# Optimization experiments

Hardware: AMD Instinct MI355X
Metric: run time of the kernel (lower is better)

The kernel has to match this reference:

```python
import jax, jax.numpy as jnp
import numpy as np

B, O, N = 8, 100, 4096
TOK_D, D, K, H = 2048, 256, 128, 8
DH = D // H
LN_EPS = 1e-5


def _ln(x, g, b):
    m = x.mean(-1, keepdims=True)
    v = ((x - m) ** 2).mean(-1, keepdims=True)
    return (x - m) * jax.lax.rsqrt(v + LN_EPS) * g + b


def setup_inputs() -> dict:
    key = jax.random.key(0)
    ks = jax.random.split(key, 16)
    s = 0.02
    return {
        "activation": jax.random.uniform(ks[0], (B, O, N), jnp.float32),
        "tokens": jax.random.normal(ks[1], (B, N, TOK_D), jnp.float32),
        "W_tok": jax.random.normal(ks[2], (TOK_D, D), jnp.float32) * s,
        "b_tok": jnp.zeros((D,), jnp.float32),
        "g_tn": jnp.ones((D,), jnp.float32),
        "bt_tn": jnp.zeros((D,), jnp.float32),
        "pool_query": jax.random.normal(ks[3], (D,), jnp.float32) * s,
        "Wq": jax.random.normal(ks[4], (D, D), jnp.float32) * s,
        "bq": jnp.zeros((D,), jnp.float32),
        "Wk": jax.random.normal(ks[5], (D, D), jnp.float32) * s,
        "bk": jnp.zeros((D,), jnp.float32),
        "Wv": jax.random.normal(ks[6], (D, D), jnp.float32) * s,
        "bv": jnp.zeros((D,), jnp.float32),
        "Wo": jax.random.normal(ks[7], (D, D), jnp.float32) * s,
        "bo": jnp.zeros((D,), jnp.float32),
        "g_pn": jnp.ones((D,), jnp.float32),
        "bt_pn": jnp.zeros((D,), jnp.float32),
        "g_on": jnp.ones((D,), jnp.float32),
        "bt_on": jnp.zeros((D,), jnp.float32),
    }


def reference(activation, tokens, W_tok, b_tok, g_tn, bt_tn, pool_query,
              Wq, bq, Wk, bk, Wv, bv, Wo, bo, g_pn, bt_pn, g_on, bt_on):
    # project + norm the shared token pool: [B, N, D]
    tp = _ln(tokens @ W_tok + b_tok, g_tn, bt_tn)

    # weighted-average branch
    w = activation / jnp.clip(activation.sum(-1, keepdims=True), 1e-8)
    weighted_avg = jnp.einsum('bon,bnd->bod', w, tp)

    # top-k attention branch
    _, topk_idx = jax.lax.top_k(activation, K)            # [B, O, K]
    topk_tokens = jax.vmap(lambda t, i: t[i])(tp, topk_idx)  # [B, O, K, D]

    # MultiheadAttention with a single shared query vector (q_len = 1)
    q = (pool_query @ Wq + bq).reshape(H, DH)             # [H, DH]
    kp = (topk_tokens @ Wk + bk).reshape(B, O, K, H, DH)
    vp = (topk_tokens @ Wv + bv).reshape(B, O, K, H, DH)
    scores = jnp.einsum('hd,bokhd->bohk', q, kp) / np.sqrt(DH).astype(np.float32)
    attn = jax.nn.softmax(scores, axis=-1)                # [B, O, H, K]
    pooled = jnp.einsum('bohk,bokhd->bohd', attn, vp).reshape(B, O, D)
    pooled = _ln(pooled @ Wo + bo, g_pn, bt_pn)

    return _ln(weighted_avg + pooled, g_on, bt_on)
```

## Files before the change

kernel.cpp:

```cpp
#include <hip/hip_runtime.h>
#include <hip/hip_bf16.h>

#define DEVI static __device__ __forceinline__

typedef __attribute__((ext_vector_type(8))) short short8;
typedef __attribute__((ext_vector_type(4))) float f32x4;

#define B_   8
#define O_   100
#define N_   4096
#define TOKD 2048
#define D_   256
#define K_   128
#define H_   8
#define M_   (B_*N_)

DEVI unsigned short f2bf(float f) {
    unsigned u = __float_as_uint(f);
    u = (u + 0x7FFFu + ((u >> 16) & 1u)) >> 16;
    return (unsigned short)u;
}
DEVI float bf2f(unsigned v) { return __uint_as_float(v << 16); }

DEVI unsigned pkbf(float lo, float hi) {
    unsigned r;
    asm("v_cvt_pk_bf16_f32 %0, %1, %2" : "=v"(r) : "v"(lo), "v"(hi));
    return r;
}
DEVI void gload16(const void* g, void* l) {
    __builtin_amdgcn_global_load_lds((const __attribute__((address_space(1))) void*)g,
                                     (__attribute__((address_space(3))) void*)l, 16, 0, 0);
}

__global__ __launch_bounds__(256) void k_pre(const float* __restrict__ act,
                                             int* __restrict__ oidx,
                                             float* __restrict__ asum,
                                             const float* __restrict__ W,
                                             unsigned short* __restrict__ wtb,
                                             const float* __restrict__ pq,
                                             const float* __restrict__ Wq,
                                             const float* __restrict__ bqv,
                                             const float* __restrict__ Wk,
                                             const float* __restrict__ bkv,
                                             float* __restrict__ qW,
                                             float* __restrict__ qb) {
    __shared__ __align__(16) char smem[50304];
    const int t = threadIdx.x, lane = t & 63, wid = t >> 6;

    if (blockIdx.x >= 800) {
        const int bx = blockIdx.x - 800;
        if (bx < 2048) {
            int idx = bx * 256 + t;
            int k = idx >> 8, n = idx & 255;
            wtb[n * TOKD + k] = f2bf(W[idx]);
            return;
        }
        float (*qpart)[32] = (float(*)[32])smem;
        float* qhl = (float*)(smem + 1024);
        const int h = bx - 2048;
        const int col = h * 32 + (t & 31), sl = t >> 5;
        float s = 0.f;
        #pragma unroll
        for (int e = 0; e < 32; ++e) s += pq[sl * 32 + e] * Wq[(sl * 32 + e) * D_ + col];
        qpart[sl][t & 31] = s;
        __syncthreads();
        if (t < 32) {
            float u = bqv[h * 32 + t];
            #pragma unroll
            for (int s8 = 0; s8 < 8; ++s8) u += qpart[s8][t];
            qhl[t] = u;
        }
        __syncthreads();
        float u = 0.f;
        #pragma unroll
        for (int dd = 0; dd < 32; ++dd) u += qhl[dd] * Wk[t * D_ + h * 32 + dd];
        qW[h * D_ + t] = u;
        if (t == 0) {
            float z = 0.f;
            for (int dd = 0; dd < 32; ++dd) z += qhl[dd] * bkv[h * 32 + dd];
            qb[h] = z;
        }
        return;
    }

    int* hist = (int*)smem;
    unsigned long long* cand = (unsigned long long*)(smem + 16384);
    int* csum = (int*)(smem + 49152);
    int* sb   = (int*)(smem + 50192);
    int* cnts = (int*)(smem + 50200);
    float* redf = (float*)(smem + 50208);
    unsigned long long* redu = (unsigned long long*)(smem + 50224);

    const int blk = blockIdx.x;
    const float* rp = act + (size_t)blk * N_;
    float fv[16]; unsigned vb[16]; int bins[16];
    float fs = 0.f;
    #pragma unroll
    for (int i = 0; i < 16; ++i) {
        float f = rp[t + i * 256];
        fv[i] = f; vb[i] = __float_as_uint(f);
        fs += f;
    }
    #pragma unroll
    for (int i = 0; i < 16; ++i) hist[t + i * 256] = 0;
    if (t == 0) { cnts[0] = 0; cnts[1] = 0; }
    #pragma unroll
    for (int m = 1; m < 64; m <<= 1) fs += __shfl_xor(fs, m);
    if (!lane) redf[wid] = fs;
    __syncthreads();
    if (t == 0) asum[blk] = fmaxf(redf[0] + redf[1] + redf[2] + redf[3], 1e-8f);

    #pragma unroll
    for (int i = 0; i < 16; ++i) {
        float f = fv[i];
        int b = (f >= 1.0f) ? 4095 : ((f > 0.f) ? (int)(f * 4096.f) : 0);
        bins[i] = b;
        atomicAdd(&hist[b], 1);
    }
    __syncthreads();

    int cs = 0;
    #pragma unroll
    for (int i = 0; i < 16; ++i) cs += hist[t * 16 + i];
    int v = cs;
    #pragma unroll
    for (int off = 1; off < 64; off <<= 1) {
        int o = __shfl_down(v, off);
        if (lane + off < 64) v += o;
    }
    if (!lane) csum[256 + wid] = v;
    __syncthreads();
    int stot = 0;
    for (int w2 = wid + 1; w2 < 4; ++w2) stot += csum[256 + w2];
    int suff = v + stot;
    csum[t] = suff;
    __syncthreads();
    int nxtc = (t < 255) ? csum[t + 1] : 0;
    if (suff >= K_ && nxtc < K_) {
        int run = nxtc, bstar = t * 16;
        for (int bi = 15; bi >= 0; --bi) {
            run += hist[t * 16 + bi];
            if (run >= K_) { bstar = t * 16 + bi; break; }
        }
        sb[0] = bstar;
    }
    __syncthreads();
    const int bstar = sb[0];

    #pragma unroll
    for (int i = 0; i < 16; ++i) {
        if (bins[i] > bstar) {
            int p = atomicAdd(&cnts[0], 1);
            oidx[blk * K_ + p] = t + i * 256;
        } else if (bins[i] == bstar) {
            int p = atomicAdd(&cnts[1], 1);
            cand[p] = ((unsigned long long)vb[i] << 16) | (unsigned)(4095 - (t + i * 256));
        }
    }
    __syncthreads();
    const int g = cnts[0], E = cnts[1], m = K_ - g;
    unsigned long long last = ~0ull;
    for (int slot = 0; slot < m; ++slot) {
        unsigned long long best = 0;
        for (int i = t; i < E; i += 256) {
            unsigned long long e = cand[i];
            if (e < last && e > best) best = e;
        }
        #pragma unroll
        for (int mm = 1; mm < 64; mm <<= 1) {
            unsigned long long o = __shfl_xor(best, mm);
            if (o > best) best = o;
        }
        if (!lane) redu[wid] = best;
        __syncthreads();
        best = redu[0];
        if (redu[1] > best) best = redu[1];
        if (redu[2] > best) best = redu[2];
        if (redu[3] > best) best = redu[3];
        if (t == 0) oidx[blk * K_ + g + slot] = 4095 - (int)(best & 0xFFFFull);
        last = best;
        __syncthreads();
    }
}

__global__ __launch_bounds__(512, 2) void k_gemm1(const float* __restrict__ A,
                                                  const unsigned short* __restrict__ Bt,
                                                  const float* __restrict__ btok,
                                                  const float* __restrict__ g,
                                                  const float* __restrict__ bt,
                                                  unsigned short* __restrict__ tp) {
    __shared__ __align__(16) char smem[98304];
    const int t = threadIdx.x;
    const int bm = blockIdx.x;
    const int lane = t & 63, w = t >> 6;
    const int wm = w >> 2, wn = w & 3;
    const int lr = lane >> 4, lc = lane & 15;

    const int arow = t >> 2;
    const int acb = (t & 3) * 32;
    const float* agp = A + (size_t)(bm * 128 + arow) * TOKD + (t & 3) * 16;
    const int aw0 = arow * 128 + (acb ^ ((arow & 7) << 4));
    const int aw1 = arow * 128 + ((acb + 16) ^ ((arow & 7) << 4));
    const unsigned short* bg = Bt + (size_t)(t >> 3) * TOKD
                        + (((((t & 7) << 4)) ^ (((t >> 3) & 7) << 4)) >> 1);
    char* bldsw = smem + 32768 + (t >> 6) * 1024;

    f32x4 acc[4][4] = {};
    const int NT = TOKD / 64;
    float4 a0, a1, a2, a3;

    a0 = *(const float4*)(agp);     a1 = *(const float4*)(agp + 4);
    a2 = *(const float4*)(agp + 8); a3 = *(const float4*)(agp + 12);
    #pragma unroll
    for (int c = 0; c < 4; ++c) gload16(bg + (size_t)c * 64 * TOKD, bldsw + c * 8192);
    {
        uint4 w0, w1;
        w0.x = pkbf(a0.x, a0.y); w0.y = pkbf(a0.z, a0.w);
        w0.z = pkbf(a1.x, a1.y); w0.w = pkbf(a1.z, a1.w);
        w1.x = pkbf(a2.x, a2.y); w1.y = pkbf(a2.z, a2.w);
        w1.z = pkbf(a3.x, a3.y); w1.w = pkbf(a3.z, a3.w);
        *(uint4*)(smem + aw0) = w0; *(uint4*)(smem + aw1) = w1;
    }
    a0 = *(const float4*)(agp + 64);  a1 = *(const float4*)(agp + 68);
    a2 = *(const float4*)(agp + 72);  a3 = *(const float4*)(agp + 76);
    asm volatile("s_waitcnt vmcnt(4) lgkmcnt(0)" ::: "memory");
    __builtin_amdgcn_s_barrier();

    int cur = 0;
    for (int kt = 0; kt < NT; ++kt) {
        const int nxt = cur ^ 1;
        if (kt + 1 < NT) {
            const unsigned short* bn = bg + (size_t)(kt + 1) * 64;
            #pragma unroll
            for (int c = 0; c < 4; ++c)
                gload16(bn + (size_t)c * 64 * TOKD, bldsw + nxt * 32768 + c * 8192);
        }
        const char* Ab = smem + cur * 16384;
        const char* Bb = smem + 32768 + cur * 32768;
        #pragma unroll
        for (int kk = 0; kk < 2; ++kk) {
            short8 afr[4], bfr[4];
            #pragma unroll
            for (int mi = 0; mi < 4; ++mi) {
                int row = wm * 64 + mi * 16 + lc;
                afr[mi] = *(const short8*)(Ab + row * 128 + ((kk * 64 + lr * 16) ^ ((row & 7) << 4)));
            }
            #pragma unroll
            for (int ni = 0; ni < 4; ++ni) {
                int n = wn * 64 + ni * 16 + lc;
                bfr[ni] = *(const short8*)(Bb + n * 128 + ((kk * 64 + lr * 16) ^ ((n & 7) << 4)));
            }
            __builtin_amdgcn_s_setprio(1);
            #pragma unroll
            for (int mi = 0; mi < 4; ++mi)
                #pragma unroll
                for (int ni = 0; ni < 4; ++ni)
                    acc[mi][ni] = __builtin_amdgcn_mfma_f32_16x16x32_bf16(afr[mi], bfr[ni], acc[mi][ni], 0, 0, 0);
            __builtin_amdgcn_s_setprio(0);
        }
        if (kt + 1 < NT) {
            char* Anw = smem + nxt * 16384;
            uint4 w0, w1;
            w0.x = pkbf(a0.x, a0.y); w0.y = pkbf(a0.z, a0.w);
            w0.z = pkbf(a1.x, a1.y); w0.w = pkbf(a1.z, a1.w);
            w1.x = pkbf(a2.x, a2.y); w1.y = pkbf(a2.z, a2.w);
            w1.z = pkbf(a3.x, a3.y); w1.w = pkbf(a3.z, a3.w);
            *(uint4*)(Anw + aw0) = w0; *(uint4*)(Anw + aw1) = w1;
            if (kt + 2 < NT) {
                const float* ap = agp + (size_t)(kt + 2) * 64;
                a0 = *(const float4*)(ap);     a1 = *(const float4*)(ap + 4);
                a2 = *(const float4*)(ap + 8); a3 = *(const float4*)(ap + 12);
                asm volatile("s_waitcnt vmcnt(4) lgkmcnt(0)" ::: "memory");
            } else {
                asm volatile("s_waitcnt vmcnt(0) lgkmcnt(0)" ::: "memory");
            }
            __builtin_amdgcn_s_barrier();
            cur = nxt;
        }
    }
    __syncthreads();

    float* ep = (float*)smem;
    const int col0 = lane * 4;
    float4 b4 = *(const float4*)(btok + col0);
    float4 g4 = *(const float4*)(g + col0);
    float4 t4 = *(const float4*)(bt + col0);
    #pragma unroll
    for (int chunk = 0; chunk < 2; ++chunk) {
        if (wm == chunk) {
            #pragma unroll
            for (int mi = 0; mi < 4; ++mi)
                #pragma unroll
                for (int ni = 0; ni < 4; ++ni)
                    #pragma unroll
                    for (int r = 0; r < 4; ++r)
                        ep[(mi * 16 + lr * 4 + r) * 260 + wn * 64 + ni * 16 + lc] = acc[mi][ni][r];
        }
        __syncthreads();
        #pragma unroll
        for (int rr = 0; rr < 8; ++rr) {
            int row = w * 8 + rr;
            float4 x4 = *(const float4*)(ep + row * 260 + col0);
            float x0 = x4.x + b4.x, x1 = x4.y + b4.y, x2 = x4.z + b4.z, x3 = x4.w + b4.w;
            float s = x0 + x1 + x2 + x3;
            float q = x0*x0 + x1*x1 + x2*x2 + x3*x3;
            #pragma unroll
            for (int m = 1; m < 64; m <<= 1) { s += __shfl_xor(s, m); q += __shfl_xor(q, m); }
            float mean = s * (1.f/256.f);
            float var = q * (1.f/256.f) - mean * mean;
            float rs = rsqrtf(var + 1e-5f);
            ushort4 o;
            o.x = f2bf((x0-mean)*rs*g4.x + t4.x);
            o.y = f2bf((x1-mean)*rs*g4.y + t4.y);
            o.z = f2bf((x2-mean)*rs*g4.z + t4.z);
            o.w = f2bf((x3-mean)*rs*g4.w + t4.w);
            *(ushort4*)(tp + (size_t)(bm * 128 + chunk * 64 + row) * D_ + col0) = o;
        }
        __syncthreads();
    }
}

__global__ __launch_bounds__(256) void k_wavg(const float* __restrict__ act,
                                              const unsigned short* __restrict__ tp,
                                              float* __restrict__ partial) {
    const int kc = blockIdx.x;
    const int b = blockIdx.y;
    const int d = threadIdx.x;
    const unsigned short* tpb = tp + ((size_t)b * N_ + kc * 128) * D_ + d;
    const float* actb = act + (size_t)b * O_ * N_ + kc * 128;
    float* pout = partial + ((size_t)(b * 32 + kc) * O_) * D_ + d;
    for (int oci = 0; oci < 2; ++oci) {
        const int oc = blockIdx.z * 2 + oci;
        float acc[10] = {};
        #pragma unroll 2
        for (int q = 0; q < 32; ++q) {
            float t0 = bf2f(tpb[(q * 4 + 0) * D_]);
            float t1 = bf2f(tpb[(q * 4 + 1) * D_]);
            float t2 = bf2f(tpb[(q * 4 + 2) * D_]);
            float t3 = bf2f(tpb[(q * 4 + 3) * D_]);
            #pragma unroll
            for (int oj = 0; oj < 10; ++oj) {
                float4 a4 = *(const float4*)(actb + (size_t)(oc * 10 + oj) * N_ + q * 4);
                acc[oj] += a4.x * t0 + a4.y * t1 + a4.z * t2 + a4.w * t3;
            }
        }
        #pragma unroll
        for (int oj = 0; oj < 10; ++oj)
            pout[(size_t)(oc * 10 + oj) * D_] = acc[oj];
    }
}

DEVI int swz(int j, int chunk) { return j * 512 + ((chunk ^ (j & 31)) << 4); }

__global__ __launch_bounds__(256) void k_attn(
    const unsigned short* __restrict__ tp, const int* __restrict__ oidx,
    const float* __restrict__ qW, const float* __restrict__ qbv,
    const float* __restrict__ Wv, const float* __restrict__ bv,
    const float* __restrict__ Wo, const float* __restrict__ bo,
    const float* __restrict__ g_pn, const float* __restrict__ bt_pn,
    const float* __restrict__ g_on, const float* __restrict__ bt_on,
    const float* __restrict__ partial, const float* __restrict__ asum,
    float* __restrict__ outp)
{
    __shared__ uint4 tgU[4096];
    __shared__ float sc[H_ * K_];
    __shared__ float ul[H_ * D_];
    __shared__ float pool_lds[D_];
    __shared__ float redf[8];
    __shared__ int idxl[K_];
    char* tg = (char*)tgU;

    const int t = threadIdx.x, lane = t & 63, wid = t >> 6;
    const int blk = blockIdx.x;
    const int b = blk / O_;
    const int o = blk - b * O_;

    if (t < K_) idxl[t] = oidx[blk * K_ + t];
    __syncthreads();

    #pragma unroll
    for (int it = 0; it < 16; ++it) {
        int c = t + it * 256;
        int j = c >> 5, ch = c & 31;
        uint4 v = *(const uint4*)(tp + ((size_t)(b * N_ + idxl[j])) * D_ + ch * 8);
        *(uint4*)(tg + swz(j, ch)) = v;
    }
    __syncthreads();

    {
        const int j = t & 127, hq = t >> 7;
        const float* q0 = qW + hq * 4 * D_;
        float s0 = 0.f, s1 = 0.f, s2 = 0.f, s3 = 0.f;
        #pragma unroll 4
        for (int e8 = 0; e8 < 32; ++e8) {
            uint4 tv = *(const uint4*)(tg + swz(j, e8));
            float f0 = bf2f(tv.x & 0xffffu), f1 = bf2f(tv.x >> 16);
            float f2 = bf2f(tv.y & 0xffffu), f3 = bf2f(tv.y >> 16);
            float f4 = bf2f(tv.z & 0xffffu), f5 = bf2f(tv.z >> 16);
            float f6 = bf2f(tv.w & 0xffffu), f7 = bf2f(tv.w >> 16);
            const float* qa = q0 + e8 * 8;
            const float* qbp = qa + D_;
            const float* qc = qa + 2 * D_;
            const float* qd = qa + 3 * D_;
            s0 += f0*qa[0]+f1*qa[1]+f2*qa[2]+f3*qa[3]+f4*qa[4]+f5*qa[5]+f6*qa[6]+f7*qa[7];
            s1 += f0*qbp[0]+f1*qbp[1]+f2*qbp[2]+f3*qbp[3]+f4*qbp[4]+f5*qbp[5]+f6*qbp[6]+f7*qbp[7];
            s2 += f0*qc[0]+f1*qc[1]+f2*qc[2]+f3*qc[3]+f4*qc[4]+f5*qc[5]+f6*qc[6]+f7*qc[7];
            s3 += f0*qd[0]+f1*qd[1]+f2*qd[2]+f3*qd[3]+f4*qd[4]+f5*qd[5]+f6*qd[6]+f7*qd[7];
        }
        const float sca = 0.1767766952966369f;
        sc[(hq * 4 + 0) * K_ + j] = (s0 + qbv[hq * 4 + 0]) * sca;
        sc[(hq * 4 + 1) * K_ + j] = (s1 + qbv[hq * 4 + 1]) * sca;
        sc[(hq * 4 + 2) * K_ + j] = (s2 + qbv[hq * 4 + 2]) * sca;
        sc[(hq * 4 + 3) * K_ + j] = (s3 + qbv[hq * 4 + 3]) * sca;
    }
    __syncthreads();

    #pragma unroll
    for (int hh = 0; hh < 2; ++hh) {
        int h = wid * 2 + hh;
        float v0 = sc[h * K_ + lane], v1 = sc[h * K_ + 64 + lane];
        float mx = fmaxf(v0, v1);
        #pragma unroll
        for (int m = 1; m < 64; m <<= 1) mx = fmaxf(mx, __shfl_xor(mx, m));
        float e0 = __expf(v0 - mx), e1 = __expf(v1 - mx);
        float ss = e0 + e1;
        #pragma unroll
        for (int m = 1; m < 64; m <<= 1) ss += __shfl_xor(ss, m);
        float inv = 1.0f / ss;
        sc[h * K_ + lane] = e0 * inv;
        sc[h * K_ + 64 + lane] = e1 * inv;
    }
    __syncthreads();

    {
        const int h = t >> 5, eg = t & 31;
        float a8[8] = {};
        #pragma unroll 2
        for (int jb = 0; jb < 32; ++jb) {
            f32x4 p4 = *(const f32x4*)(sc + h * K_ + jb * 4);
            #pragma unroll
            for (int ji = 0; ji < 4; ++ji) {
                int j = jb * 4 + ji;
                uint4 tv = *(const uint4*)(tg + swz(j, eg));
                float pw = p4[ji];
                a8[0] += pw * bf2f(tv.x & 0xffffu); a8[1] += pw * bf2f(tv.x >> 16);
                a8[2] += pw * bf2f(tv.y & 0xffffu); a8[3] += pw * bf2f(tv.y >> 16);
                a8[4] += pw * bf2f(tv.z & 0xffffu); a8[5] += pw * bf2f(tv.z >> 16);
                a8[6] += pw * bf2f(tv.w & 0xffffu); a8[7] += pw * bf2f(tv.w >> 16);
            }
        }
        #pragma unroll
        for (int i = 0; i < 8; ++i) ul[h * D_ + eg * 8 + i] = a8[i];
    }
    __syncthreads();

    {
        int h = t >> 5;
        const float* up = ul + h * D_;
        float p = bv[t];
        #pragma unroll 8
        for (int e = 0; e < D_; ++e) p += up[e] * Wv[e * D_ + t];
        pool_lds[t] = p;
    }
    __syncthreads();
    float po = bo[t];
    #pragma unroll 8
    for (int e = 0; e < D_; ++e) po += pool_lds[e] * Wo[e * D_ + t];

    float s1 = po, q1 = po * po;
    #pragma unroll
    for (int m = 1; m < 64; m <<= 1) { s1 += __shfl_xor(s1, m); q1 += __shfl_xor(q1, m); }
    if (!lane) { redf[wid] = s1; redf[4 + wid] = q1; }
    __syncthreads();
    s1 = redf[0] + redf[1] + redf[2] + redf[3];
    q1 = redf[4] + redf[5] + redf[6] + redf[7];
    float mean = s1 * (1.f/256.f);
    float var = q1 * (1.f/256.f) - mean * mean;
    float rs = rsqrtf(var + 1e-5f);
    float pl = (po - mean) * rs * g_pn[t] + bt_pn[t];
    __syncthreads();

    float wa = 0.f;
    const float* pp = partial + ((size_t)(b * 32) * O_ + o) * D_ + t;
    #pragma unroll 8
    for (int kc = 0; kc < 32; ++kc) wa += pp[(size_t)kc * O_ * D_];
    float x = wa / asum[blk] + pl;
    float s2 = x, q2 = x * x;
    #pragma unroll
    for (int m = 1; m < 64; m <<= 1) { s2 += __shfl_xor(s2, m); q2 += __shfl_xor(q2, m); }
    if (!lane) { redf[wid] = s2; redf[4 + wid] = q2; }
    __syncthreads();
    s2 = redf[0] + redf[1] + redf[2] + redf[3];
    q2 = redf[4] + redf[5] + redf[6] + redf[7];
    float mean2 = s2 * (1.f/256.f);
    float var2 = q2 * (1.f/256.f) - mean2 * mean2;
    float rs2 = rsqrtf(var2 + 1e-5f);
    outp[(size_t)blk * D_ + t] = (x - mean2) * rs2 * g_on[t] + bt_on[t];
}

extern "C" void kernel_launch(void* const* d_in, const int* in_sizes, int n_in,
                              void* d_out, int out_size, void* d_ws, size_t ws_size,
                              hipStream_t stream) {
    const float* act    = (const float*)d_in[0];
    const float* tokens = (const float*)d_in[1];
    const float* W_tok  = (const float*)d_in[2];
    const float* b_tok  = (const float*)d_in[3];
    const float* g_tn   = (const float*)d_in[4];
    const float* bt_tn  = (const float*)d_in[5];
    const float* pq     = (const float*)d_in[6];
    const float* Wq     = (const float*)d_in[7];
    const float* bq     = (const float*)d_in[8];
    const float* Wk     = (const float*)d_in[9];
    const float* bk     = (const float*)d_in[10];
    const float* Wv     = (const float*)d_in[11];
    const float* bv     = (const float*)d_in[12];
    const float* Wo     = (const float*)d_in[13];
    const float* bo     = (const float*)d_in[14];
    const float* g_pn   = (const float*)d_in[15];
    const float* bt_pn  = (const float*)d_in[16];
    const float* g_on   = (const float*)d_in[17];
    const float* bt_on  = (const float*)d_in[18];

    char* ws = (char*)d_ws;
    unsigned short* wtb   = (unsigned short*)ws;
    unsigned short* tp    = (unsigned short*)(ws + 1048576);
    int*   tidx = (int*)(ws + 17825792);
    float* asum = (float*)(ws + 18235392);
    float* part = (float*)(ws + 18238592);
    float* qW   = (float*)(ws + 44452992);
    float* qb   = (float*)(ws + 44461184);

    k_pre<<<2856, 256, 0, stream>>>(act, tidx, asum, W_tok, wtb,
                                    pq, Wq, bq, Wk, bk, qW, qb);
    k_gemm1<<<M_ / 128, 512, 0, stream>>>(tokens, wtb, b_tok, g_tn, bt_tn, tp);
    k_wavg<<<dim3(32, 8, 5), 256, 0, stream>>>(act, tp, part);
    k_attn<<<B_ * O_, 256, 0, stream>>>(tp, tidx, qW, qb, Wv, bv, Wo, bo,
                                        g_pn, bt_pn, g_on, bt_on, part, asum,
                                        (float*)d_out);
}
```

Measured before the change: 226.1 us.

## Retile token-projection GEMM to 64-row blocks with K-step 32 and new LDS layout

The token projection GEMM moves from 128x256 tiles with 512 threads and K-step 64 to 64x256 tiles with 256 threads and K-step 32. Each wave now owns a 64x64 output slab across all rows, and the swizzled LDS layout is replaced with a k-chunk-major layout. The aim is more blocks (512 instead of 256) for better CU coverage, less LDS per block, and a single-pass LayerNorm epilogue. In exchange, each B tile is reused by fewer rows, so the weight matrix is read from global memory twice as often, and there are twice as many barriered K iterations. The unswizzled layout may also cause LDS bank conflicts.

```diff
diff --git a/kernel.cpp b/kernel.cpp
--- a/kernel.cpp
+++ b/kernel.cpp
@@ -183,94 +183,74 @@
     }
 }
 
-__global__ __launch_bounds__(512, 2) void k_gemm1(const float* __restrict__ A,
+__global__ __launch_bounds__(256, 2) void k_gemm1(const float* __restrict__ A,
                                                   const unsigned short* __restrict__ Bt,
                                                   const float* __restrict__ btok,
                                                   const float* __restrict__ g,
                                                   const float* __restrict__ bt,
                                                   unsigned short* __restrict__ tp) {
-    __shared__ __align__(16) char smem[98304];
+    __shared__ __align__(16) char smem[66560];
     const int t = threadIdx.x;
     const int bm = blockIdx.x;
     const int lane = t & 63, w = t >> 6;
-    const int wm = w >> 2, wn = w & 3;
     const int lr = lane >> 4, lc = lane & 15;
 
-    const int arow = t >> 2;
-    const int acb = (t & 3) * 32;
-    const float* agp = A + (size_t)(bm * 128 + arow) * TOKD + (t & 3) * 16;
-    const int aw0 = arow * 128 + (acb ^ ((arow & 7) << 4));
-    const int aw1 = arow * 128 + ((acb + 16) ^ ((arow & 7) << 4));
-    const unsigned short* bg = Bt + (size_t)(t >> 3) * TOKD
-                        + (((((t & 7) << 4)) ^ (((t >> 3) & 7) << 4)) >> 1);
-    char* bldsw = smem + 32768 + (t >> 6) * 1024;
+    const float* agp = A + (size_t)(bm * 64 + (t >> 2)) * TOKD + (t & 3) * 8;
+    const int awo = (t & 3) * 1024 + (t >> 2) * 16;
+    const unsigned short* bg = Bt + (size_t)t * TOKD;
+    char* bldw = smem + 8192 + (w << 10);
 
     f32x4 acc[4][4] = {};
-    const int NT = TOKD / 64;
-    float4 a0, a1, a2, a3;
-
-    a0 = *(const float4*)(agp);     a1 = *(const float4*)(agp + 4);
-    a2 = *(const float4*)(agp + 8); a3 = *(const float4*)(agp + 12);
-    #pragma unroll
-    for (int c = 0; c < 4; ++c) gload16(bg + (size_t)c * 64 * TOKD, bldsw + c * 8192);
+    const int NT = TOKD / 32;
+    float4 a0, a1;
+
+    a0 = *(const float4*)(agp); a1 = *(const float4*)(agp + 4);
     {
-        uint4 w0, w1;
+        uint4 w0;
         w0.x = pkbf(a0.x, a0.y); w0.y = pkbf(a0.z, a0.w);
         w0.z = pkbf(a1.x, a1.y); w0.w = pkbf(a1.z, a1.w);
-        w1.x = pkbf(a2.x, a2.y); w1.y = pkbf(a2.z, a2.w);
-        w1.z = pkbf(a3.x, a3.y); w1.w = pkbf(a3.z, a3.w);
-        *(uint4*)(smem + aw0) = w0; *(uint4*)(smem + aw1) = w1;
-    }
-    a0 = *(const float4*)(agp + 64);  a1 = *(const float4*)(agp + 68);
-    a2 = *(const float4*)(agp + 72);  a3 = *(const float4*)(agp + 76);
-    asm volatile("s_waitcnt vmcnt(4) lgkmcnt(0)" ::: "memory");
+        *(uint4*)(smem + awo) = w0;
+    }
+    #pragma unroll
+    for (int c = 0; c < 4; ++c) gload16(bg + c * 8, bldw + c * 4096);
+    a0 = *(const float4*)(agp + 32); a1 = *(const float4*)(agp + 36);
+    asm volatile("s_waitcnt vmcnt(2) lgkmcnt(0)" ::: "memory");
     __builtin_amdgcn_s_barrier();
 
     int cur = 0;
     for (int kt = 0; kt < NT; ++kt) {
         const int nxt = cur ^ 1;
         if (kt + 1 < NT) {
-            const unsigned short* bn = bg + (size_t)(kt + 1) * 64;
+            const unsigned short* bn = bg + (kt + 1) * 32;
+            char* dst = bldw + nxt * 16384;
             #pragma unroll
-            for (int c = 0; c < 4; ++c)
-                gload16(bn + (size_t)c * 64 * TOKD, bldsw + nxt * 32768 + c * 8192);
-        }
-        const char* Ab = smem + cur * 16384;
-        const char* Bb = smem + 32768 + cur * 32768;
-        #pragma unroll
-        for (int kk = 0; kk < 2; ++kk) {
-            short8 afr[4], bfr[4];
+            for (int c = 0; c < 4; ++c) gload16(bn + c * 8, dst + c * 4096);
+        }
+        const char* Ab = smem + cur * 4096;
+        const char* Bb = smem + 8192 + cur * 16384;
+        short8 afr[4], bfr[4];
+        #pragma unroll
+        for (int mi = 0; mi < 4; ++mi)
+            afr[mi] = *(const short8*)(Ab + lr * 1024 + (mi * 16 + lc) * 16);
+        #pragma unroll
+        for (int ni = 0; ni < 4; ++ni)
+            bfr[ni] = *(const short8*)(Bb + lr * 4096 + (w * 64 + ni * 16 + lc) * 16);
+        __builtin_amdgcn_s_setprio(1);
+        #pragma unroll
+        for (int mi = 0; mi < 4; ++mi)
             #pragma unroll
-            for (int mi = 0; mi < 4; ++mi) {
-                int row = wm * 64 + mi * 16 + lc;
-                afr[mi] = *(const short8*)(Ab + row * 128 + ((kk * 64 + lr * 16) ^ ((row & 7) << 4)));
-            }
-            #pragma unroll
-            for (int ni = 0; ni < 4; ++ni) {
-                int n = wn * 64 + ni * 16 + lc;
-                bfr[ni] = *(const short8*)(Bb + n * 128 + ((kk * 64 + lr * 16) ^ ((n & 7) << 4)));
-            }
-            __builtin_amdgcn_s_setprio(1);
-            #pragma unroll
-            for (int mi = 0; mi < 4; ++mi)
-                #pragma unroll
-                for (int ni = 0; ni < 4; ++ni)
-                    acc[mi][ni] = __builtin_amdgcn_mfma_f32_16x16x32_bf16(afr[mi], bfr[ni], acc[mi][ni], 0, 0, 0);
-            __builtin_amdgcn_s_setprio(0);
-        }
+            for (int ni = 0; ni < 4; ++ni)
+                acc[mi][ni] = __builtin_amdgcn_mfma_f32_16x16x32_bf16(afr[mi], bfr[ni], acc[mi][ni], 0, 0, 0);
+        __builtin_amdgcn_s_setprio(0);
         if (kt + 1 < NT) {
-            char* Anw = smem + nxt * 16384;
-            uint4 w0, w1;
+            uint4 w0;
             w0.x = pkbf(a0.x, a0.y); w0.y = pkbf(a0.z, a0.w);
             w0.z = pkbf(a1.x, a1.y); w0.w = pkbf(a1.z, a1.w);
-            w1.x = pkbf(a2.x, a2.y); w1.y = pkbf(a2.z, a2.w);
-            w1.z = pkbf(a3.x, a3.y); w1.w = pkbf(a3.z, a3.w);
-            *(uint4*)(Anw + aw0) = w0; *(uint4*)(Anw + aw1) = w1;
+            *(uint4*)(smem + nxt * 4096 + awo) = w0;
             if (kt + 2 < NT) {
-                const float* ap = agp + (size_t)(kt + 2) * 64;
-                a0 = *(const float4*)(ap);     a1 = *(const float4*)(ap + 4);
-                a2 = *(const float4*)(ap + 8); a3 = *(const float4*)(ap + 12);
-                asm volatile("s_waitcnt vmcnt(4) lgkmcnt(0)" ::: "memory");
+                const float* ap = agp + (size_t)(kt + 2) * 32;
+                a0 = *(const float4*)(ap); a1 = *(const float4*)(ap + 4);
+                asm volatile("s_waitcnt vmcnt(2) lgkmcnt(0)" ::: "memory");
             } else {
                 asm volatile("s_waitcnt vmcnt(0) lgkmcnt(0)" ::: "memory");
             }
@@ -286,37 +266,31 @@
     float4 g4 = *(const float4*)(g + col0);
     float4 t4 = *(const float4*)(bt + col0);
     #pragma unroll
-    for (int chunk = 0; chunk < 2; ++chunk) {
-        if (wm == chunk) {
+    for (int mi = 0; mi < 4; ++mi)
+        #pragma unroll
+        for (int ni = 0; ni < 4; ++ni)
             #pragma unroll
-            for (int mi = 0; mi < 4; ++mi)
-                #pragma unroll
-                for (int ni = 0; ni < 4; ++ni)
-                    #pragma unroll
-                    for (int r = 0; r < 4; ++r)
-                        ep[(mi * 16 + lr * 4 + r) * 260 + wn * 64 + ni * 16 + lc] = acc[mi][ni][r];
-        }
-        __syncthreads();
-        #pragma unroll
-        for (int rr = 0; rr < 8; ++rr) {
-            int row = w * 8 + rr;
-            float4 x4 = *(const float4*)(ep + row * 260 + col0);
-            float x0 = x4.x + b4.x, x1 = x4.y + b4.y, x2 = x4.z + b4.z, x3 = x4.w + b4.w;
-            float s = x0 + x1 + x2 + x3;
-            float q = x0*x0 + x1*x1 + x2*x2 + x3*x3;
-            #pragma unroll
-            for (int m = 1; m < 64; m <<= 1) { s += __shfl_xor(s, m); q += __shfl_xor(q, m); }
-            float mean = s * (1.f/256.f);
-            float var = q * (1.f/256.f) - mean * mean;
-            float rs = rsqrtf(var + 1e-5f);
-            ushort4 o;
-            o.x = f2bf((x0-mean)*rs*g4.x + t4.x);
-            o.y = f2bf((x1-mean)*rs*g4.y + t4.y);
-            o.z = f2bf((x2-mean)*rs*g4.z + t4.z);
-            o.w = f2bf((x3-mean)*rs*g4.w + t4.w);
-            *(ushort4*)(tp + (size_t)(bm * 128 + chunk * 64 + row) * D_ + col0) = o;
-        }
-        __syncthreads();
+            for (int r = 0; r < 4; ++r)
+                ep[(mi * 16 + lr * 4 + r) * 260 + w * 64 + ni * 16 + lc] = acc[mi][ni][r];
+    __syncthreads();
+    #pragma unroll
+    for (int rr = 0; rr < 16; ++rr) {
+        int row = w * 16 + rr;
+        float4 x4 = *(const float4*)(ep + row * 260 + col0);
+        float x0 = x4.x + b4.x, x1 = x4.y + b4.y, x2 = x4.z + b4.z, x3 = x4.w + b4.w;
+        float s = x0 + x1 + x2 + x3;
+        float q = x0*x0 + x1*x1 + x2*x2 + x3*x3;
+        #pragma unroll
+        for (int m = 1; m < 64; m <<= 1) { s += __shfl_xor(s, m); q += __shfl_xor(q, m); }
+        float mean = s * (1.f/256.f);
+        float var = q * (1.f/256.f) - mean * mean;
+        float rs = rsqrtf(var + 1e-5f);
+        ushort4 o;
+        o.x = f2bf((x0-mean)*rs*g4.x + t4.x);
+        o.y = f2bf((x1-mean)*rs*g4.y + t4.y);
+        o.z = f2bf((x2-mean)*rs*g4.z + t4.z);
+        o.w = f2bf((x3-mean)*rs*g4.w + t4.w);
+        *(ushort4*)(tp + (size_t)(bm * 64 + row) * D_ + col0) = o;
     }
 }
 
@@ -532,7 +506,7 @@
 
     k_pre<<<2856, 256, 0, stream>>>(act, tidx, asum, W_tok, wtb,
                                     pq, Wq, bq, Wk, bk, qW, qb);
-    k_gemm1<<<M_ / 128, 512, 0, stream>>>(tokens, wtb, b_tok, g_tn, bt_tn, tp);
+    k_gemm1<<<M_ / 64, 256, 0, stream>>>(tokens, wtb, b_tok, g_tn, bt_tn, tp);
     k_wavg<<<dim3(32, 8, 5), 256, 0, stream>>>(act, tp, part);
     k_attn<<<B_ * O_, 256, 0, stream>>>(tp, tidx, qW, qb, Wv, bv, Wo, bo,
                                         g_pn, bt_pn, g_on, bt_on, part, asum,
```

New measurement: 285.5 us. 26.3% more time.
